# Optimization experiments

Measured on AMD Instinct MI355X. Metric: run time of the kernel, lower is better.

The kernel has to match this reference:

```python
import jax, jax.numpy as jnp
import numpy as np

# Multi-scale spatial shapes for a 704x256 input at strides 4/8/16/32
LEVEL_SHAPES = [(64, 176), (32, 88), (16, 44), (8, 22)]  # sum HW = 14960
NUM_CAMS, NUM_LEVELS, NUM_PTS, NUM_GROUPS = 6, 4, 13, 8
NUM_ANCHOR, EMBED_DIMS = 900, 256


def setup_inputs() -> dict:
    key = jax.random.key(0)
    ks = jax.random.split(key, 8)
    total_hw = sum(h * w for h, w in LEVEL_SHAPES)
    feat = jax.random.normal(ks[0], (1, NUM_CAMS, total_hw, EMBED_DIMS), jnp.float32)
    key_points = jax.random.uniform(ks[1], (1, NUM_ANCHOR, NUM_PTS, 3), jnp.float32)
    # near-identity projection so sampled locations spread over the image plane
    lidar2img = jnp.eye(4, dtype=jnp.float32)[None, None] + 0.05 * jax.random.normal(
        ks[2], (1, NUM_CAMS, 4, 4), jnp.float32)
    image_wh = jnp.ones((1, NUM_CAMS, 2), jnp.float32)
    instance_feature = jax.random.normal(ks[3], (1, NUM_ANCHOR, EMBED_DIMS), jnp.float32)
    anchor_embed = jax.random.normal(ks[4], (1, NUM_ANCHOR, EMBED_DIMS), jnp.float32)
    k_out = NUM_CAMS * NUM_LEVELS * NUM_PTS * NUM_GROUPS  # 2496
    weights_fc_w = jax.random.normal(ks[5], (k_out, EMBED_DIMS), jnp.float32) * 0.02
    weights_fc_b = jnp.zeros((k_out,), jnp.float32)
    out_proj_w = jax.random.normal(ks[6], (EMBED_DIMS, EMBED_DIMS), jnp.float32) * 0.02
    out_proj_b = jnp.zeros((EMBED_DIMS,), jnp.float32)
    return dict(feat=feat, key_points=key_points, lidar2img=lidar2img, image_wh=image_wh,
                instance_feature=instance_feature, anchor_embed=anchor_embed,
                weights_fc_w=weights_fc_w, weights_fc_b=weights_fc_b,
                out_proj_w=out_proj_w, out_proj_b=out_proj_b)


def _bilinear_sample(feat_flat, H, W, loc):
    # feat_flat: [bs, cams, H*W, C]; loc: [bs, cams, Q, 2] normalized to [0,1]
    x = loc[..., 0] * W - 0.5
    y = loc[..., 1] * H - 0.5
    x0 = jnp.floor(x); y0 = jnp.floor(y)
    wx1 = x - x0; wy1 = y - y0
    x0i = x0.astype(jnp.int32); y0i = y0.astype(jnp.int32)
    acc = jnp.zeros(loc.shape[:-1] + (feat_flat.shape[-1],), feat_flat.dtype)
    for dx, dy, w in ((0, 0, (1 - wx1) * (1 - wy1)), (1, 0, wx1 * (1 - wy1)),
                      (0, 1, (1 - wx1) * wy1), (1, 1, wx1 * wy1)):
        xi = x0i + dx; yi = y0i + dy
        valid = ((xi >= 0) & (xi < W) & (yi >= 0) & (yi < H)).astype(feat_flat.dtype)
        idx = jnp.clip(yi, 0, H - 1) * W + jnp.clip(xi, 0, W - 1)  # [bs, cams, Q]
        g = jnp.take_along_axis(feat_flat, idx[..., None], axis=2)  # [bs, cams, Q, C]
        acc = acc + g * (w * valid)[..., None]
    return acc


def reference(feat, key_points, lidar2img, image_wh, instance_feature, anchor_embed,
              weights_fc_w, weights_fc_b, out_proj_w, out_proj_b):
    bs, A, P = key_points.shape[:3]
    C, G, L, Ncam = EMBED_DIMS, NUM_GROUPS, NUM_LEVELS, NUM_CAMS
    # ---- _get_weights: fc + softmax over (cams*levels*pts) per group ----
    logits = jnp.einsum('bad,kd->bak', instance_feature + anchor_embed, weights_fc_w) + weights_fc_b
    w = jax.nn.softmax(logits.reshape(bs, A, -1, G), axis=-2)
    w = w.reshape(bs, A, Ncam, L, P, G).transpose(0, 1, 4, 2, 3, 5)  # [bs,A,P,cams,L,G]
    # ---- project_points ----
    pts_h = jnp.concatenate([key_points, jnp.ones_like(key_points[..., :1])], axis=-1)  # [bs,A,P,4]
    proj = jnp.einsum('bcij,bapj->bcapi', lidar2img, pts_h)  # [bs,cams,A,P,4]
    xy = proj[..., :2] / jnp.clip(proj[..., 2:3], 1e-5, None)
    pts2d = xy / image_wh[:, :, None, None, :]               # [bs,cams,A,P,2]
    loc = pts2d.reshape(bs, Ncam, A * P, 2)
    # ---- DAF: per-level bilinear sample + group-weighted reduction ----
    out_acc = jnp.zeros((bs, A, G, C // G), feat.dtype)
    start = 0
    for li, (H, W) in enumerate(LEVEL_SHAPES):
        fl = feat[:, :, start:start + H * W, :]
        s = _bilinear_sample(fl, H, W, loc)                   # [bs,cams,A*P,C]
        s = s.reshape(bs, Ncam, A, P, G, C // G)
        out_acc = out_acc + jnp.einsum('bapcg,bcapgd->bagd', w[..., li, :], s)
        start += H * W
    features = out_acc.reshape(bs, A, C)
    return features @ out_proj_w.T + out_proj_b  # output_proj
```

## Files before the change

kernel.cpp:

```cpp
#include <hip/hip_runtime.h>
#include <math.h>

#define EMBED   256
#define NCAM    6
#define NLVL    4
#define NPTS    13
#define NGRP    8
#define NANCH   900
#define NTERM   (NCAM*NLVL*NPTS)
#define KOUT    (NTERM*NGRP)
#define TOTHW   14960

__global__ __launch_bounds__(256)
void gemm_bias_f32(const float* __restrict__ A0, const float* __restrict__ A1,
                   const float* __restrict__ B,  const float* __restrict__ bias,
                   float* __restrict__ Cout, int M, int N, int K)
{
    const int BM = 64, BN = 64, BK = 32;
    __shared__ float As[32][64 + 1];
    __shared__ float Bs[32][64 + 1];

    const int bm = blockIdx.y * BM;
    const int bn = blockIdx.x * BN;
    const int tid = threadIdx.x;
    const int tx = tid & 15;
    const int ty = tid >> 4;

    float acc[4][4] = {{0.f}};

    for (int k0 = 0; k0 < K; k0 += BK) {
        #pragma unroll
        for (int i = 0; i < 2; ++i) {
            int lin = (tid + i * 256) * 4;
            int r = lin >> 5;
            int cc = lin & 31;
            int gm = bm + r;
            float4 v = make_float4(0.f, 0.f, 0.f, 0.f);
            if (gm < M) {
                v = *reinterpret_cast<const float4*>(A0 + (size_t)gm * K + k0 + cc);
                if (A1) {
                    float4 v1 = *reinterpret_cast<const float4*>(A1 + (size_t)gm * K + k0 + cc);
                    v.x += v1.x; v.y += v1.y; v.z += v1.z; v.w += v1.w;
                }
            }
            As[cc + 0][r] = v.x; As[cc + 1][r] = v.y;
            As[cc + 2][r] = v.z; As[cc + 3][r] = v.w;
        }
        #pragma unroll
        for (int i = 0; i < 2; ++i) {
            int lin = (tid + i * 256) * 4;
            int r = lin >> 5;
            int cc = lin & 31;
            int gn = bn + r;
            float4 v = make_float4(0.f, 0.f, 0.f, 0.f);
            if (gn < N) {
                v = *reinterpret_cast<const float4*>(B + (size_t)gn * K + k0 + cc);
            }
            Bs[cc + 0][r] = v.x; Bs[cc + 1][r] = v.y;
            Bs[cc + 2][r] = v.z; Bs[cc + 3][r] = v.w;
        }
        __syncthreads();

        #pragma unroll
        for (int k = 0; k < BK; ++k) {
            float a[4], b[4];
            #pragma unroll
            for (int i = 0; i < 4; ++i) a[i] = As[k][ty * 4 + i];
            #pragma unroll
            for (int j = 0; j < 4; ++j) b[j] = Bs[k][tx * 4 + j];
            #pragma unroll
            for (int i = 0; i < 4; ++i)
                #pragma unroll
                for (int j = 0; j < 4; ++j)
                    acc[i][j] = fmaf(a[i], b[j], acc[i][j]);
        }
        __syncthreads();
    }

    #pragma unroll
    for (int i = 0; i < 4; ++i) {
        int m = bm + ty * 4 + i;
        if (m >= M) break;
        #pragma unroll
        for (int j = 0; j < 4; ++j) {
            int n = bn + tx * 4 + j;
            if (n < N) Cout[(size_t)m * N + n] = acc[i][j] + (bias ? bias[n] : 0.f);
        }
    }
}

__global__ __launch_bounds__(256)
void sample_agg(const float* __restrict__ feat,
                const float* __restrict__ key_points,
                const float* __restrict__ lidar2img,
                const float* __restrict__ image_wh,
                const float* __restrict__ logits,
                float* __restrict__ outacc)
{
    __shared__ alignas(16) float wl[KOUT];
    __shared__ alignas(16) int   cidx[NTERM][4];
    __shared__ alignas(16) float cwgt[NTERM][4];
    __shared__ int tmap[NTERM];
    __shared__ int ncomp;

    const int a   = blockIdx.x;
    const int tid = threadIdx.x;

    if (tid == 0) ncomp = 0;

    {
        const float4* src = reinterpret_cast<const float4*>(logits + (size_t)a * KOUT);
        float4* dst = reinterpret_cast<float4*>(wl);
        for (int i = tid; i < KOUT / 4; i += 256) dst[i] = src[i];
    }
    __syncthreads();

    {
        int g = tid >> 5;
        int j = tid & 31;
        float mx = -1e30f;
        for (int m = j; m < NTERM; m += 32) mx = fmaxf(mx, wl[m * NGRP + g]);
        #pragma unroll
        for (int s = 16; s > 0; s >>= 1) mx = fmaxf(mx, __shfl_xor(mx, s, 32));
        float sum = 0.f;
        for (int m = j; m < NTERM; m += 32) {
            float e = __expf(wl[m * NGRP + g] - mx);
            wl[m * NGRP + g] = e;
            sum += e;
        }
        #pragma unroll
        for (int s = 16; s > 0; s >>= 1) sum += __shfl_xor(sum, s, 32);
        float inv = 1.f / sum;
        for (int m = j; m < NTERM; m += 32) wl[m * NGRP + g] *= inv;
    }

    for (int t = tid; t < NTERM; t += 256) {
        int cam = t / (NLVL * NPTS);
        int rem = t - cam * (NLVL * NPTS);
        int lvl = rem / NPTS;
        int p   = rem - lvl * NPTS;

        const float* kp = key_points + ((size_t)a * NPTS + p) * 3;
        float px = kp[0], py = kp[1], pz = kp[2];
        const float* M4 = lidar2img + cam * 16;
        float X = M4[0] * px + M4[1] * py + M4[2]  * pz + M4[3];
        float Y = M4[4] * px + M4[5] * py + M4[6]  * pz + M4[7];
        float Z = M4[8] * px + M4[9] * py + M4[10] * pz + M4[11];
        float zc = fmaxf(Z, 1e-5f);
        float u = (X / zc) / image_wh[cam * 2 + 0];
        float v = (Y / zc) / image_wh[cam * 2 + 1];

        int H = 64 >> lvl, W = 176 >> lvl;
        int st = (lvl == 0) ? 0 : (lvl == 1) ? 11264 : (lvl == 2) ? 14080 : 14784;

        float x = u * (float)W - 0.5f;
        float y = v * (float)H - 0.5f;
        float x0f = floorf(x), y0f = floorf(y);
        float wx1 = x - x0f, wy1 = y - y0f;
        float wx0 = 1.f - wx1, wy0 = 1.f - wy1;
        int x0 = (int)x0f, y0 = (int)y0f;
        int x1 = x0 + 1,   y1 = y0 + 1;

        bool vx0 = (x0 >= 0) & (x0 < W), vx1 = (x1 >= 0) & (x1 < W);
        bool vy0 = (y0 >= 0) & (y0 < H), vy1 = (y1 >= 0) & (y1 < H);
        int cx0 = min(max(x0, 0), W - 1), cx1 = min(max(x1, 0), W - 1);
        int cy0 = min(max(y0, 0), H - 1), cy1 = min(max(y1, 0), H - 1);

        float w00 = wx0 * wy0 * ((vx0 & vy0) ? 1.f : 0.f);
        float w10 = wx1 * wy0 * ((vx1 & vy0) ? 1.f : 0.f);
        float w01 = wx0 * wy1 * ((vx0 & vy1) ? 1.f : 0.f);
        float w11 = wx1 * wy1 * ((vx1 & vy1) ? 1.f : 0.f);

        if ((w00 != 0.f) | (w10 != 0.f) | (w01 != 0.f) | (w11 != 0.f)) {
            int slot = atomicAdd(&ncomp, 1);
            int base = cam * TOTHW + st;
            cidx[slot][0] = base + cy0 * W + cx0;
            cidx[slot][1] = base + cy0 * W + cx1;
            cidx[slot][2] = base + cy1 * W + cx0;
            cidx[slot][3] = base + cy1 * W + cx1;
            cwgt[slot][0] = w00;
            cwgt[slot][1] = w10;
            cwgt[slot][2] = w01;
            cwgt[slot][3] = w11;
            tmap[slot] = t;
        }
    }
    __syncthreads();

    const int c = tid;
    const int g = c >> 5;
    const int nt = ncomp;
    float acc = 0.f;
    const float* fbase = feat + c;

    #pragma unroll 4
    for (int s = 0; s < nt; ++s) {
        int4   I  = *reinterpret_cast<const int4*>(&cidx[s][0]);
        float4 Wt = *reinterpret_cast<const float4*>(&cwgt[s][0]);
        float  gw = wl[tmap[s] * NGRP + g];
        float v0 = fbase[(size_t)I.x * EMBED];
        float v1 = fbase[(size_t)I.y * EMBED];
        float v2 = fbase[(size_t)I.z * EMBED];
        float v3 = fbase[(size_t)I.w * EMBED];
        float sv = v0 * Wt.x + v1 * Wt.y + v2 * Wt.z + v3 * Wt.w;
        acc = fmaf(sv, gw, acc);
    }
    outacc[(size_t)a * EMBED + c] = acc;
}

extern "C" void kernel_launch(void* const* d_in, const int* in_sizes, int n_in,
                              void* d_out, int out_size, void* d_ws, size_t ws_size,
                              hipStream_t stream)
{
    const float* feat   = (const float*)d_in[0];
    const float* kp     = (const float*)d_in[1];
    const float* l2i    = (const float*)d_in[2];
    const float* iwh    = (const float*)d_in[3];
    const float* inst   = (const float*)d_in[4];
    const float* anch   = (const float*)d_in[5];
    const float* wfc    = (const float*)d_in[6];
    const float* bfc    = (const float*)d_in[7];
    const float* wproj  = (const float*)d_in[8];
    const float* bproj  = (const float*)d_in[9];
    float* out = (float*)d_out;

    float* logits = (float*)d_ws;
    float* outacc = logits + (size_t)NANCH * KOUT;

    {
        dim3 grid(KOUT / 64, (NANCH + 63) / 64);
        gemm_bias_f32<<<grid, 256, 0, stream>>>(inst, anch, wfc, bfc,
                                                logits, NANCH, KOUT, EMBED);
    }

    sample_agg<<<dim3(NANCH), 256, 0, stream>>>(feat, kp, l2i, iwh, logits, outacc);

    {
        dim3 grid(EMBED / 64, (NANCH + 63) / 64);
        gemm_bias_f32<<<grid, 256, 0, stream>>>(outacc, nullptr, wproj, bproj,
                                                out, NANCH, EMBED, EMBED);
    }
}
```

Baseline: 252.6 us.

## Split sampling kernel across term chunks with separate softmax and atomic accumulation

Moves the softmax into its own kernel that writes normalized weights to workspace and zeroes the accumulator. The sampling/aggregation kernel is split four ways per anchor (3600 blocks) so each block handles a quarter of the camera/level/point terms, with partial sums combined by float atomicAdd. Feature offsets are premultiplied by EMBED, and the GEMM loads are merged into one loop with float4 shared-memory reads. This adds parallelism and shortens each block's serial gather chain, at the cost of an extra launch, extra global traffic for the weights, atomics, and non-deterministic summation order.

```diff
diff --git a/kernel.cpp b/kernel.cpp
--- a/kernel.cpp
+++ b/kernel.cpp
@@ -10,18 +10,20 @@
 #define NTERM   (NCAM*NLVL*NPTS)
 #define KOUT    (NTERM*NGRP)
 #define TOTHW   14960
+#define SPLIT   4
+#define TPS     (NTERM/SPLIT)
 
 __global__ __launch_bounds__(256)
 void gemm_bias_f32(const float* __restrict__ A0, const float* __restrict__ A1,
                    const float* __restrict__ B,  const float* __restrict__ bias,
                    float* __restrict__ Cout, int M, int N, int K)
 {
-    const int BM = 64, BN = 64, BK = 32;
-    __shared__ float As[32][64 + 1];
-    __shared__ float Bs[32][64 + 1];
-
-    const int bm = blockIdx.y * BM;
-    const int bn = blockIdx.x * BN;
+    const int BK = 32;
+    __shared__ alignas(16) float As[32][68];
+    __shared__ alignas(16) float Bs[32][68];
+
+    const int bm = blockIdx.y * 64;
+    const int bn = blockIdx.x * 64;
     const int tid = threadIdx.x;
     const int tx = tid & 15;
     const int ty = tid >> 4;
@@ -45,29 +47,23 @@
             }
             As[cc + 0][r] = v.x; As[cc + 1][r] = v.y;
             As[cc + 2][r] = v.z; As[cc + 3][r] = v.w;
-        }
-        #pragma unroll
-        for (int i = 0; i < 2; ++i) {
-            int lin = (tid + i * 256) * 4;
-            int r = lin >> 5;
-            int cc = lin & 31;
+
             int gn = bn + r;
-            float4 v = make_float4(0.f, 0.f, 0.f, 0.f);
+            float4 w = make_float4(0.f, 0.f, 0.f, 0.f);
             if (gn < N) {
-                v = *reinterpret_cast<const float4*>(B + (size_t)gn * K + k0 + cc);
+                w = *reinterpret_cast<const float4*>(B + (size_t)gn * K + k0 + cc);
             }
-            Bs[cc + 0][r] = v.x; Bs[cc + 1][r] = v.y;
-            Bs[cc + 2][r] = v.z; Bs[cc + 3][r] = v.w;
+            Bs[cc + 0][r] = w.x; Bs[cc + 1][r] = w.y;
+            Bs[cc + 2][r] = w.z; Bs[cc + 3][r] = w.w;
         }
         __syncthreads();
 
         #pragma unroll
         for (int k = 0; k < BK; ++k) {
-            float a[4], b[4];
-            #pragma unroll
-            for (int i = 0; i < 4; ++i) a[i] = As[k][ty * 4 + i];
-            #pragma unroll
-            for (int j = 0; j < 4; ++j) b[j] = Bs[k][tx * 4 + j];
+            float4 a4 = *reinterpret_cast<const float4*>(&As[k][ty * 4]);
+            float4 b4 = *reinterpret_cast<const float4*>(&Bs[k][tx * 4]);
+            float a[4] = {a4.x, a4.y, a4.z, a4.w};
+            float b[4] = {b4.x, b4.y, b4.z, b4.w};
             #pragma unroll
             for (int i = 0; i < 4; ++i)
                 #pragma unroll
@@ -90,23 +86,13 @@
 }
 
 __global__ __launch_bounds__(256)
-void sample_agg(const float* __restrict__ feat,
-                const float* __restrict__ key_points,
-                const float* __restrict__ lidar2img,
-                const float* __restrict__ image_wh,
-                const float* __restrict__ logits,
-                float* __restrict__ outacc)
+void softmax_k(const float* __restrict__ logits,
+               float* __restrict__ wsm,
+               float* __restrict__ outacc)
 {
     __shared__ alignas(16) float wl[KOUT];
-    __shared__ alignas(16) int   cidx[NTERM][4];
-    __shared__ alignas(16) float cwgt[NTERM][4];
-    __shared__ int tmap[NTERM];
-    __shared__ int ncomp;
-
     const int a   = blockIdx.x;
     const int tid = threadIdx.x;
-
-    if (tid == 0) ncomp = 0;
 
     {
         const float4* src = reinterpret_cast<const float4*>(logits + (size_t)a * KOUT);
@@ -115,26 +101,62 @@
     }
     __syncthreads();
 
-    {
-        int g = tid >> 5;
-        int j = tid & 31;
-        float mx = -1e30f;
-        for (int m = j; m < NTERM; m += 32) mx = fmaxf(mx, wl[m * NGRP + g]);
-        #pragma unroll
-        for (int s = 16; s > 0; s >>= 1) mx = fmaxf(mx, __shfl_xor(mx, s, 32));
-        float sum = 0.f;
-        for (int m = j; m < NTERM; m += 32) {
-            float e = __expf(wl[m * NGRP + g] - mx);
-            wl[m * NGRP + g] = e;
-            sum += e;
-        }
-        #pragma unroll
-        for (int s = 16; s > 0; s >>= 1) sum += __shfl_xor(sum, s, 32);
-        float inv = 1.f / sum;
-        for (int m = j; m < NTERM; m += 32) wl[m * NGRP + g] *= inv;
-    }
-
-    for (int t = tid; t < NTERM; t += 256) {
+    int g = tid >> 5;
+    int j = tid & 31;
+    float mx = -1e30f;
+    for (int m = j; m < NTERM; m += 32) mx = fmaxf(mx, wl[m * NGRP + g]);
+    #pragma unroll
+    for (int s = 16; s > 0; s >>= 1) mx = fmaxf(mx, __shfl_xor(mx, s, 32));
+    float sum = 0.f;
+    for (int m = j; m < NTERM; m += 32) {
+        float e = __expf(wl[m * NGRP + g] - mx);
+        wl[m * NGRP + g] = e;
+        sum += e;
+    }
+    #pragma unroll
+    for (int s = 16; s > 0; s >>= 1) sum += __shfl_xor(sum, s, 32);
+    float inv = 1.f / sum;
+    for (int m = j; m < NTERM; m += 32) wl[m * NGRP + g] *= inv;
+    __syncthreads();
+
+    {
+        const float4* src = reinterpret_cast<const float4*>(wl);
+        float4* dst = reinterpret_cast<float4*>(wsm + (size_t)a * KOUT);
+        for (int i = tid; i < KOUT / 4; i += 256) dst[i] = src[i];
+    }
+    outacc[(size_t)a * EMBED + tid] = 0.f;
+}
+
+__global__ __launch_bounds__(256)
+void sample_agg_split(const float* __restrict__ feat,
+                      const float* __restrict__ key_points,
+                      const float* __restrict__ lidar2img,
+                      const float* __restrict__ image_wh,
+                      const float* __restrict__ wsm,
+                      float* __restrict__ outacc)
+{
+    __shared__ alignas(16) float wl[TPS * NGRP];
+    __shared__ alignas(16) int   cidx[TPS][4];
+    __shared__ alignas(16) float cwgt[TPS][4];
+    __shared__ int tmap[TPS];
+    __shared__ int ncomp;
+
+    const int bid = blockIdx.x;
+    const int a   = bid >> 2;
+    const int sp  = bid & (SPLIT - 1);
+    const int t0  = sp * TPS;
+    const int tid = threadIdx.x;
+
+    if (tid == 0) ncomp = 0;
+    {
+        const float4* src = reinterpret_cast<const float4*>(wsm + (size_t)a * KOUT + t0 * NGRP);
+        float4* dst = reinterpret_cast<float4*>(wl);
+        if (tid < TPS * NGRP / 4) dst[tid] = src[tid];
+    }
+    __syncthreads();
+
+    if (tid < TPS) {
+        int t = t0 + tid;
         int cam = t / (NLVL * NPTS);
         int rem = t - cam * (NLVL * NPTS);
         int lvl = rem / NPTS;
@@ -174,15 +196,15 @@
         if ((w00 != 0.f) | (w10 != 0.f) | (w01 != 0.f) | (w11 != 0.f)) {
             int slot = atomicAdd(&ncomp, 1);
             int base = cam * TOTHW + st;
-            cidx[slot][0] = base + cy0 * W + cx0;
-            cidx[slot][1] = base + cy0 * W + cx1;
-            cidx[slot][2] = base + cy1 * W + cx0;
-            cidx[slot][3] = base + cy1 * W + cx1;
+            cidx[slot][0] = (base + cy0 * W + cx0) * EMBED;
+            cidx[slot][1] = (base + cy0 * W + cx1) * EMBED;
+            cidx[slot][2] = (base + cy1 * W + cx0) * EMBED;
+            cidx[slot][3] = (base + cy1 * W + cx1) * EMBED;
             cwgt[slot][0] = w00;
             cwgt[slot][1] = w10;
             cwgt[slot][2] = w01;
             cwgt[slot][3] = w11;
-            tmap[slot] = t;
+            tmap[slot] = tid;
         }
     }
     __syncthreads();
@@ -198,14 +220,14 @@
         int4   I  = *reinterpret_cast<const int4*>(&cidx[s][0]);
         float4 Wt = *reinterpret_cast<const float4*>(&cwgt[s][0]);
         float  gw = wl[tmap[s] * NGRP + g];
-        float v0 = fbase[(size_t)I.x * EMBED];
-        float v1 = fbase[(size_t)I.y * EMBED];
-        float v2 = fbase[(size_t)I.z * EMBED];
-        float v3 = fbase[(size_t)I.w * EMBED];
+        float v0 = fbase[I.x];
+        float v1 = fbase[I.y];
+        float v2 = fbase[I.z];
+        float v3 = fbase[I.w];
         float sv = v0 * Wt.x + v1 * Wt.y + v2 * Wt.z + v3 * Wt.w;
         acc = fmaf(sv, gw, acc);
     }
-    outacc[(size_t)a * EMBED + c] = acc;
+    atomicAdd(&outacc[(size_t)a * EMBED + c], acc);
 }
 
 extern "C" void kernel_launch(void* const* d_in, const int* in_sizes, int n_in,
@@ -225,7 +247,8 @@
     float* out = (float*)d_out;
 
     float* logits = (float*)d_ws;
-    float* outacc = logits + (size_t)NANCH * KOUT;
+    float* wsm    = logits + (size_t)NANCH * KOUT;
+    float* outacc = wsm    + (size_t)NANCH * KOUT;
 
     {
         dim3 grid(KOUT / 64, (NANCH + 63) / 64);
@@ -233,7 +256,10 @@
                                                 logits, NANCH, KOUT, EMBED);
     }
 
-    sample_agg<<<dim3(NANCH), 256, 0, stream>>>(feat, kp, l2i, iwh, logits, outacc);
+    softmax_k<<<dim3(NANCH), 256, 0, stream>>>(logits, wsm, outacc);
+
+    sample_agg_split<<<dim3(NANCH * SPLIT), 256, 0, stream>>>(feat, kp, l2i, iwh,
+                                                              wsm, outacc);
 
     {
         dim3 grid(EMBED / 64, (NANCH + 63) / 64);
```

New measurement: 235.6 us. 1.07x faster.
